# Optimization experiments

Measured on AMD Instinct MI355X. Metric: run time of the kernel, lower is better.

## Reference

```python
import jax, jax.numpy as jnp
import numpy as np

N_NODES = 50000


def _gcn_norm(edge_index, num_nodes):
    # add self-loops (PyG GCNConv default)
    loop = jnp.arange(num_nodes, dtype=edge_index.dtype)
    src = jnp.concatenate([edge_index[0], loop])
    dst = jnp.concatenate([edge_index[1], loop])
    deg = jax.ops.segment_sum(jnp.ones_like(dst, dtype=jnp.float32), dst,
                              num_segments=num_nodes)
    dis = jnp.where(deg > 0, jax.lax.rsqrt(deg), 0.0)  # deg^{-1/2}
    norm = dis[src] * dis[dst]                          # [E+N]
    return src, dst, norm


def _gcn_conv(x, W, b, src, dst, norm, num_nodes):
    h = x @ W                                   # [N, out] transform first
    msg = h[src] * norm[:, None]                # gather + scale  [E+N, out]
    out = jax.ops.segment_sum(msg, dst, num_segments=num_nodes)  # scatter-add
    return out + b


def setup_inputs() -> dict:
    key = jax.random.key(0)
    k1, k2, k3, k4, k5 = jax.random.split(key, 5)
    in_dim, hid_dim, out_dim = 128, 64, 2
    x = jax.random.normal(k1, (N_NODES, in_dim), dtype=jnp.float32)
    edge_index = jax.random.randint(k2, (2, 800000), 0, N_NODES, dtype=jnp.int64)
    s1 = 1.0 / np.sqrt(in_dim)
    s2 = 1.0 / np.sqrt(hid_dim)
    W1 = jax.random.uniform(k3, (in_dim, hid_dim), jnp.float32, -s1, s1)
    b1 = jnp.zeros((hid_dim,), jnp.float32)
    W2 = jax.random.uniform(k4, (hid_dim, hid_dim), jnp.float32, -s2, s2)
    b2 = jnp.zeros((hid_dim,), jnp.float32)
    Wl = jax.random.uniform(k5, (hid_dim, out_dim), jnp.float32, -s2, s2)
    bl = jnp.zeros((out_dim,), jnp.float32)
    return {"x": x, "edge_index": edge_index, "W1": W1, "b1": b1,
            "W2": W2, "b2": b2, "Wl": Wl, "bl": bl}


def reference(x, edge_index, W1, b1, W2, b2, Wl, bl):
    num_nodes = x.shape[0]
    src, dst, norm = _gcn_norm(edge_index, num_nodes)
    h = _gcn_conv(x, W1, b1, src, dst, norm, num_nodes)
    h = jax.nn.relu(h)
    # dropout is identity at inference
    h = _gcn_conv(h, W2, b2, src, dst, norm, num_nodes)
    h = jax.nn.relu(h)
    logits = h @ Wl + bl
    return logits
```

## Files before the change

### kernel.cpp

```cpp
#include <hip/hip_runtime.h>

#define IN_DIM 128
#define HID 64
#define STAGE_CAP 12288

__global__ __launch_bounds__(256) void k_bin_count(const int* __restrict__ dst, int E,
                                                   int* __restrict__ bcnt) {
    __shared__ int h[256];
    int tid = threadIdx.x;
    h[tid] = 0;
    __syncthreads();
    int base = blockIdx.x * 4096;
    int end = min(base + 4096, E);
    for (int i = base + tid; i < end; i += 256) atomicAdd(&h[dst[i] >> 8], 1);
    __syncthreads();
    if (h[tid]) atomicAdd(&bcnt[tid], h[tid]);
}

__global__ __launch_bounds__(256) void k_bucket_scan(const int* __restrict__ bcnt,
                                                     int* __restrict__ bbase,
                                                     int* __restrict__ gcur,
                                                     int* __restrict__ row_start, int N, int E) {
    int tid = threadIdx.x, lane = tid & 63, wid = tid >> 6;
    int v = bcnt[tid], orig = v;
    for (int off = 1; off < 64; off <<= 1) {
        int t = __shfl_up(v, off);
        if (lane >= off) v += t;
    }
    __shared__ int ws[4];
    if (lane == 63) ws[wid] = v;
    __syncthreads();
    int woff = 0;
    for (int w = 0; w < wid; ++w) woff += ws[w];
    bbase[tid] = woff + v - orig;
    gcur[tid] = 0;
    if (tid == 0) row_start[N] = E;
    if (tid == 0) bbase[256] = E;
}

__global__ __launch_bounds__(512) void k_bin_scatter(const int* __restrict__ src,
                                                     const int* __restrict__ dst, int E,
                                                     const int* __restrict__ bbase,
                                                     int* __restrict__ gcur,
                                                     unsigned* __restrict__ ebuf) {
    __shared__ int hist[256];
    __shared__ int gbase[256];
    int tid = threadIdx.x;
    for (int i = tid; i < 256; i += 512) hist[i] = 0;
    __syncthreads();
    int base = blockIdx.x * 4096;
    int pk[8], bkt[8], rnk[8];
#pragma unroll
    for (int i = 0; i < 8; ++i) {
        int e = base + tid + i * 512;
        if (e < E) {
            int s = src[e];
            int d = dst[e];
            bkt[i] = d >> 8;
            pk[i] = ((d & 255) << 16) | s;
            rnk[i] = atomicAdd(&hist[bkt[i]], 1);
        } else {
            bkt[i] = -1;
        }
    }
    __syncthreads();
    for (int b = tid; b < 256; b += 512) {
        int c = hist[b];
        if (c > 0) gbase[b] = bbase[b] + atomicAdd(&gcur[b], c);
    }
    __syncthreads();
#pragma unroll
    for (int i = 0; i < 8; ++i) {
        if (bkt[i] >= 0) ebuf[gbase[bkt[i]] + rnk[i]] = (unsigned)pk[i];
    }
}

__global__ __launch_bounds__(512) void k_bin_sort(const unsigned* __restrict__ ebuf,
                                                  const int* __restrict__ bbase, int N, int E,
                                                  int* __restrict__ row_start,
                                                  float* __restrict__ dis,
                                                  int* __restrict__ csr_src) {
    __shared__ int ldeg[256];
    __shared__ int loff[256];
    __shared__ int lcur[256];
    __shared__ int wsum[8];
    __shared__ unsigned short stage[STAGE_CAP];
    int tid = threadIdx.x;
    int node0 = blockIdx.x << 8;
    int nnode = min(256, N - node0);
    for (int i = tid; i < 256; i += 512) {
        ldeg[i] = 0;
        lcur[i] = 0;
    }
    __syncthreads();
    int bstart = bbase[blockIdx.x];
    int bend = bbase[blockIdx.x + 1];
    int cnt = bend - bstart;
    for (int i = tid; i < cnt; i += 512) {
        unsigned u = ebuf[bstart + i];
        atomicAdd(&ldeg[(u >> 16) & 255], 1);
    }
    __syncthreads();
    int lane = tid & 63, wid = tid >> 6;
    int v = 0, orig = 0;
    if (tid < 256) {
        orig = ldeg[tid];
        v = orig;
    }
    for (int off = 1; off < 64; off <<= 1) {
        int t = __shfl_up(v, off);
        if (lane >= off) v += t;
    }
    if (lane == 63) wsum[wid] = v;
    __syncthreads();
    if (tid < 256) {
        int woff = 0;
        for (int w = 0; w < wid && w < 4; ++w) woff += wsum[w];
        int excl = woff + v - orig;
        loff[tid] = excl;
        if (tid < nnode) {
            row_start[node0 + tid] = bstart + excl;
            dis[node0 + tid] = rsqrtf((float)(orig + 1));
        }
    }
    __syncthreads();
    if (cnt <= STAGE_CAP) {
        for (int i = tid; i < cnt; i += 512) {
            unsigned u = ebuf[bstart + i];
            int dlo = (u >> 16) & 255;
            int pos = loff[dlo] + atomicAdd(&lcur[dlo], 1);
            stage[pos] = (unsigned short)(u & 0xFFFF);
        }
        __syncthreads();
        for (int i = tid; i < cnt; i += 512) csr_src[bstart + i] = (int)stage[i];
    } else {
        for (int i = tid; i < cnt; i += 512) {
            unsigned u = ebuf[bstart + i];
            int dlo = (u >> 16) & 255;
            int pos = bstart + loff[dlo] + atomicAdd(&lcur[dlo], 1);
            csr_src[pos] = (int)(u & 0xFFFF);
        }
    }
}

template <int K>
__global__ __launch_bounds__(256) void k_gemm_scale(const float* __restrict__ X,
                                                    const float* __restrict__ W,
                                                    const float* __restrict__ dis, int N,
                                                    float* __restrict__ out) {
    constexpr int KP = K + 4;
    constexpr int KC = K / 4;
    __shared__ float Xs[64 * KP];
    __shared__ float Ws[K * 64];
    int tid = threadIdx.x;
    int row0 = blockIdx.x * 64;

    const float4* Wg = (const float4*)W;
    float4* Ws4 = (float4*)Ws;
    for (int i = tid; i < K * 16; i += 256) Ws4[i] = Wg[i];
    const float4* Xg = (const float4*)X;
    for (int c = tid; c < 64 * KC; c += 256) {
        int r = c / KC, k4 = c % KC;
        int row = row0 + r;
        float4 vv = make_float4(0.f, 0.f, 0.f, 0.f);
        if (row < N) vv = Xg[(size_t)row * KC + k4];
        *(float4*)&Xs[r * KP + k4 * 4] = vv;
    }
    __syncthreads();

    int cg = tid & 15;
    int rg = tid >> 4;
    float acc[4][4] = {};
#pragma unroll 2
    for (int k = 0; k < K; k += 4) {
        float4 w0 = *(float4*)&Ws[(k + 0) * 64 + cg * 4];
        float4 w1 = *(float4*)&Ws[(k + 1) * 64 + cg * 4];
        float4 w2 = *(float4*)&Ws[(k + 2) * 64 + cg * 4];
        float4 w3 = *(float4*)&Ws[(k + 3) * 64 + cg * 4];
#pragma unroll
        for (int i = 0; i < 4; ++i) {
            float4 xv = *(float4*)&Xs[(rg * 4 + i) * KP + k];
            acc[i][0] += xv.x * w0.x + xv.y * w1.x + xv.z * w2.x + xv.w * w3.x;
            acc[i][1] += xv.x * w0.y + xv.y * w1.y + xv.z * w2.y + xv.w * w3.y;
            acc[i][2] += xv.x * w0.z + xv.y * w1.z + xv.z * w2.z + xv.w * w3.z;
            acc[i][3] += xv.x * w0.w + xv.y * w1.w + xv.z * w2.w + xv.w * w3.w;
        }
    }
#pragma unroll
    for (int i = 0; i < 4; ++i) {
        int row = row0 + rg * 4 + i;
        if (row < N) {
            float s = dis[row];
            *(float4*)&out[(size_t)row * 64 + cg * 4] =
                make_float4(acc[i][0] * s, acc[i][1] * s, acc[i][2] * s, acc[i][3] * s);
        }
    }
}

__global__ __launch_bounds__(256) void k_aggregate(const float* __restrict__ Hs,
                                                   const int* __restrict__ row_start,
                                                   const int* __restrict__ csr_src,
                                                   const float* __restrict__ dis,
                                                   const float* __restrict__ bias, int N,
                                                   float* __restrict__ out) {
    const float4* Hs4 = (const float4*)Hs;
    int wave = threadIdx.x >> 6, lane = threadIdx.x & 63;
    int node = blockIdx.x * 4 + wave;
    if (node >= N) return;
    int t = lane & 7, g = lane >> 3;
    float4 a0 = make_float4(0.f, 0.f, 0.f, 0.f);
    float4 a1 = a0;
    if (g == 0) {
        a0 = Hs4[(size_t)node * 16 + t];
        a1 = Hs4[(size_t)node * 16 + t + 8];
    }
    int e0 = row_start[node], e1 = row_start[node + 1];
    for (int eb = e0; eb < e1; eb += 64) {
        int cnt = min(64, e1 - eb);
        int sv = (eb + lane < e1) ? csr_src[eb + lane] : 0;
        for (int jb = 0; jb < cnt; jb += 16) {
            int i0 = jb + g, i1 = jb + 8 + g;
            int s0 = __shfl(sv, i0 < cnt ? i0 : 0);
            int s1 = __shfl(sv, i1 < cnt ? i1 : 0);
            size_t b0 = (size_t)s0 * 16, b1 = (size_t)s1 * 16;
            float4 z00 = Hs4[b0 + t];
            float4 z01 = Hs4[b0 + t + 8];
            float4 z10 = Hs4[b1 + t];
            float4 z11 = Hs4[b1 + t + 8];
            if (i0 < cnt) {
                a0.x += z00.x; a0.y += z00.y; a0.z += z00.z; a0.w += z00.w;
                a1.x += z01.x; a1.y += z01.y; a1.z += z01.z; a1.w += z01.w;
            }
            if (i1 < cnt) {
                a0.x += z10.x; a0.y += z10.y; a0.z += z10.z; a0.w += z10.w;
                a1.x += z11.x; a1.y += z11.y; a1.z += z11.z; a1.w += z11.w;
            }
        }
    }
#pragma unroll
    for (int off = 8; off < 64; off <<= 1) {
        a0.x += __shfl_xor(a0.x, off); a0.y += __shfl_xor(a0.y, off);
        a0.z += __shfl_xor(a0.z, off); a0.w += __shfl_xor(a0.w, off);
        a1.x += __shfl_xor(a1.x, off); a1.y += __shfl_xor(a1.y, off);
        a1.z += __shfl_xor(a1.z, off); a1.w += __shfl_xor(a1.w, off);
    }
    float sc = dis[node];
    const float4* b4 = (const float4*)bias;
    float4 b0 = b4[t], b1 = b4[t + 8];
    float4 v0, v1;
    v0.x = fmaxf(a0.x * sc + b0.x, 0.f); v0.y = fmaxf(a0.y * sc + b0.y, 0.f);
    v0.z = fmaxf(a0.z * sc + b0.z, 0.f); v0.w = fmaxf(a0.w * sc + b0.w, 0.f);
    v1.x = fmaxf(a1.x * sc + b1.x, 0.f); v1.y = fmaxf(a1.y * sc + b1.y, 0.f);
    v1.z = fmaxf(a1.z * sc + b1.z, 0.f); v1.w = fmaxf(a1.w * sc + b1.w, 0.f);
    if (g == 0) {
        float4* o4 = (float4*)out;
        o4[(size_t)node * 16 + t] = v0;
        o4[(size_t)node * 16 + t + 8] = v1;
    }
}

__global__ __launch_bounds__(256) void k_aggregate_head(const float* __restrict__ Hs,
                                                        const int* __restrict__ row_start,
                                                        const int* __restrict__ csr_src,
                                                        const float* __restrict__ dis,
                                                        const float* __restrict__ bias,
                                                        const float* __restrict__ Wl,
                                                        const float* __restrict__ bl, int N,
                                                        float* __restrict__ out) {
    const float4* Hs4 = (const float4*)Hs;
    int wave = threadIdx.x >> 6, lane = threadIdx.x & 63;
    int node = blockIdx.x * 4 + wave;
    if (node >= N) return;
    int t = lane & 7, g = lane >> 3;
    float4 a0 = make_float4(0.f, 0.f, 0.f, 0.f);
    float4 a1 = a0;
    if (g == 0) {
        a0 = Hs4[(size_t)node * 16 + t];
        a1 = Hs4[(size_t)node * 16 + t + 8];
    }
    int e0 = row_start[node], e1 = row_start[node + 1];
    for (int eb = e0; eb < e1; eb += 64) {
        int cnt = min(64, e1 - eb);
        int sv = (eb + lane < e1) ? csr_src[eb + lane] : 0;
        for (int jb = 0; jb < cnt; jb += 16) {
            int i0 = jb + g, i1 = jb + 8 + g;
            int s0 = __shfl(sv, i0 < cnt ? i0 : 0);
            int s1 = __shfl(sv, i1 < cnt ? i1 : 0);
            size_t b0 = (size_t)s0 * 16, b1 = (size_t)s1 * 16;
            float4 z00 = Hs4[b0 + t];
            float4 z01 = Hs4[b0 + t + 8];
            float4 z10 = Hs4[b1 + t];
            float4 z11 = Hs4[b1 + t + 8];
            if (i0 < cnt) {
                a0.x += z00.x; a0.y += z00.y; a0.z += z00.z; a0.w += z00.w;
                a1.x += z01.x; a1.y += z01.y; a1.z += z01.z; a1.w += z01.w;
            }
            if (i1 < cnt) {
                a0.x += z10.x; a0.y += z10.y; a0.z += z10.z; a0.w += z10.w;
                a1.x += z11.x; a1.y += z11.y; a1.z += z11.z; a1.w += z11.w;
            }
        }
    }
#pragma unroll
    for (int off = 8; off < 64; off <<= 1) {
        a0.x += __shfl_xor(a0.x, off); a0.y += __shfl_xor(a0.y, off);
        a0.z += __shfl_xor(a0.z, off); a0.w += __shfl_xor(a0.w, off);
        a1.x += __shfl_xor(a1.x, off); a1.y += __shfl_xor(a1.y, off);
        a1.z += __shfl_xor(a1.z, off); a1.w += __shfl_xor(a1.w, off);
    }
    float sc = dis[node];
    const float4* b4 = (const float4*)bias;
    float4 b0 = b4[t], b1 = b4[t + 8];
    float4 v0, v1;
    v0.x = fmaxf(a0.x * sc + b0.x, 0.f); v0.y = fmaxf(a0.y * sc + b0.y, 0.f);
    v0.z = fmaxf(a0.z * sc + b0.z, 0.f); v0.w = fmaxf(a0.w * sc + b0.w, 0.f);
    v1.x = fmaxf(a1.x * sc + b1.x, 0.f); v1.y = fmaxf(a1.y * sc + b1.y, 0.f);
    v1.z = fmaxf(a1.z * sc + b1.z, 0.f); v1.w = fmaxf(a1.w * sc + b1.w, 0.f);
    int c0 = 4 * t, c1 = 32 + 4 * t;
    float p0 = v0.x * Wl[(c0 + 0) * 2] + v0.y * Wl[(c0 + 1) * 2] +
               v0.z * Wl[(c0 + 2) * 2] + v0.w * Wl[(c0 + 3) * 2] +
               v1.x * Wl[(c1 + 0) * 2] + v1.y * Wl[(c1 + 1) * 2] +
               v1.z * Wl[(c1 + 2) * 2] + v1.w * Wl[(c1 + 3) * 2];
    float p1 = v0.x * Wl[(c0 + 0) * 2 + 1] + v0.y * Wl[(c0 + 1) * 2 + 1] +
               v0.z * Wl[(c0 + 2) * 2 + 1] + v0.w * Wl[(c0 + 3) * 2 + 1] +
               v1.x * Wl[(c1 + 0) * 2 + 1] + v1.y * Wl[(c1 + 1) * 2 + 1] +
               v1.z * Wl[(c1 + 2) * 2 + 1] + v1.w * Wl[(c1 + 3) * 2 + 1];
    p0 += __shfl_xor(p0, 1); p1 += __shfl_xor(p1, 1);
    p0 += __shfl_xor(p0, 2); p1 += __shfl_xor(p1, 2);
    p0 += __shfl_xor(p0, 4); p1 += __shfl_xor(p1, 4);
    if (lane == 0) {
        out[node * 2 + 0] = p0 + bl[0];
        out[node * 2 + 1] = p1 + bl[1];
    }
}

extern "C" void kernel_launch(void* const* d_in, const int* in_sizes, int n_in,
                              void* d_out, int out_size, void* d_ws, size_t ws_size,
                              hipStream_t stream) {
    const float* x  = (const float*)d_in[0];
    const int*   ei = (const int*)d_in[1];
    const float* W1 = (const float*)d_in[2];
    const float* b1 = (const float*)d_in[3];
    const float* W2 = (const float*)d_in[4];
    const float* b2 = (const float*)d_in[5];
    const float* Wl = (const float*)d_in[6];
    const float* bl = (const float*)d_in[7];

    const int N = in_sizes[0] / IN_DIM;
    const int E = in_sizes[1] / 2;
    const int* src = ei;
    const int* dst = ei + E;

    char* ws = (char*)d_ws;
    size_t off = 0;
    auto alloc = [&](size_t bytes) -> void* {
        void* p = ws + off;
        off = (off + bytes + 255) & ~(size_t)255;
        return p;
    };
    int*   bcnt      = (int*)alloc(256 * 4);
    int*   bbase     = (int*)alloc(257 * 4);
    int*   gcur      = (int*)alloc(256 * 4);
    int*   row_start = (int*)alloc(((size_t)N + 1) * 4);
    float* dis       = (float*)alloc((size_t)N * 4);
    int*   csr_src   = (int*)alloc((size_t)E * 4);
    float* bufA      = (float*)alloc((size_t)N * HID * 4);
    float* bufB      = (float*)alloc((size_t)N * HID * 4);
    unsigned* ebuf   = (unsigned*)bufA;

    hipMemsetAsync(bcnt, 0, 256 * 4, stream);

    int eblk = (E + 4095) / 4096;
    int nb = (N + 255) / 256;
    k_bin_count<<<eblk, 256, 0, stream>>>(dst, E, bcnt);
    k_bucket_scan<<<1, 256, 0, stream>>>(bcnt, bbase, gcur, row_start, N, E);
    k_bin_scatter<<<eblk, 512, 0, stream>>>(src, dst, E, bbase, gcur, ebuf);
    k_bin_sort<<<nb, 512, 0, stream>>>(ebuf, bbase, N, E, row_start, dis, csr_src);

    int gblk = (N + 63) / 64;
    int nblk = (N + 3) / 4;
    k_gemm_scale<IN_DIM><<<gblk, 256, 0, stream>>>(x, W1, dis, N, bufA);
    k_aggregate<<<nblk, 256, 0, stream>>>(bufA, row_start, csr_src, dis, b1, N, bufB);
    k_gemm_scale<HID><<<gblk, 256, 0, stream>>>(bufB, W2, dis, N, bufA);
    k_aggregate_head<<<nblk, 256, 0, stream>>>(bufA, row_start, csr_src, dis, b2, Wl, bl, N,
                                               (float*)d_out);
}
```

Measured before the change: 135.1 us.

## Overlap first-layer GEMM with CSR build by co-scheduling blocks in preprocessing kernels

Removes the dis scaling from the first GEMM so it no longer waits on the degree computation. Its tiles are split across the histogram, scan and scatter kernels, running in spare blocks alongside the edge binning. The per-source normalization moves into the aggregation loop via a gathered dis[src] multiply. The change also replaces the memset and global atomics for the bin count with a per-block 2D histogram, and unrolls aggregation to 4 neighbors per step. In exchange, the aggregation does an extra dis gather per edge, the scan block serially sums eblk rows, and the fused kernels carry larger shared memory.

```diff
diff --git a/kernel.cpp b/kernel.cpp
--- a/kernel.cpp
+++ b/kernel.cpp
@@ -3,75 +3,152 @@
 #define IN_DIM 128
 #define HID 64
 #define STAGE_CAP 12288
-
-__global__ __launch_bounds__(256) void k_bin_count(const int* __restrict__ dst, int E,
-                                                   int* __restrict__ bcnt) {
-    __shared__ int h[256];
+#define SMEM_FLOATS (64 * (IN_DIM + 4) + IN_DIM * 64)
+
+template <int K>
+__device__ __forceinline__ void gemm_body(const float* __restrict__ X,
+                                          const float* __restrict__ W, int N,
+                                          float* __restrict__ out, int blk, float* smem) {
+    constexpr int KP = K + 4;
+    constexpr int KC = K / 4;
+    float* Xs = smem;
+    float* Ws = smem + 64 * KP;
     int tid = threadIdx.x;
-    h[tid] = 0;
+    int row0 = blk * 64;
+
+    const float4* Wg = (const float4*)W;
+    float4* Ws4 = (float4*)Ws;
+    for (int i = tid; i < K * 16; i += 256) Ws4[i] = Wg[i];
+    const float4* Xg = (const float4*)X;
+    for (int c = tid; c < 64 * KC; c += 256) {
+        int r = c / KC, k4 = c % KC;
+        int row = row0 + r;
+        float4 vv = make_float4(0.f, 0.f, 0.f, 0.f);
+        if (row < N) vv = Xg[(size_t)row * KC + k4];
+        *(float4*)&Xs[r * KP + k4 * 4] = vv;
+    }
     __syncthreads();
-    int base = blockIdx.x * 4096;
-    int end = min(base + 4096, E);
-    for (int i = base + tid; i < end; i += 256) atomicAdd(&h[dst[i] >> 8], 1);
-    __syncthreads();
-    if (h[tid]) atomicAdd(&bcnt[tid], h[tid]);
-}
-
-__global__ __launch_bounds__(256) void k_bucket_scan(const int* __restrict__ bcnt,
-                                                     int* __restrict__ bbase,
-                                                     int* __restrict__ gcur,
-                                                     int* __restrict__ row_start, int N, int E) {
-    int tid = threadIdx.x, lane = tid & 63, wid = tid >> 6;
-    int v = bcnt[tid], orig = v;
-    for (int off = 1; off < 64; off <<= 1) {
-        int t = __shfl_up(v, off);
-        if (lane >= off) v += t;
-    }
-    __shared__ int ws[4];
-    if (lane == 63) ws[wid] = v;
-    __syncthreads();
-    int woff = 0;
-    for (int w = 0; w < wid; ++w) woff += ws[w];
-    bbase[tid] = woff + v - orig;
-    gcur[tid] = 0;
-    if (tid == 0) row_start[N] = E;
-    if (tid == 0) bbase[256] = E;
-}
-
-__global__ __launch_bounds__(512) void k_bin_scatter(const int* __restrict__ src,
-                                                     const int* __restrict__ dst, int E,
-                                                     const int* __restrict__ bbase,
-                                                     int* __restrict__ gcur,
-                                                     unsigned* __restrict__ ebuf) {
-    __shared__ int hist[256];
-    __shared__ int gbase[256];
-    int tid = threadIdx.x;
-    for (int i = tid; i < 256; i += 512) hist[i] = 0;
-    __syncthreads();
-    int base = blockIdx.x * 4096;
-    int pk[8], bkt[8], rnk[8];
-#pragma unroll
-    for (int i = 0; i < 8; ++i) {
-        int e = base + tid + i * 512;
-        if (e < E) {
-            int s = src[e];
-            int d = dst[e];
-            bkt[i] = d >> 8;
-            pk[i] = ((d & 255) << 16) | s;
-            rnk[i] = atomicAdd(&hist[bkt[i]], 1);
-        } else {
-            bkt[i] = -1;
-        }
-    }
-    __syncthreads();
-    for (int b = tid; b < 256; b += 512) {
-        int c = hist[b];
-        if (c > 0) gbase[b] = bbase[b] + atomicAdd(&gcur[b], c);
-    }
-    __syncthreads();
-#pragma unroll
-    for (int i = 0; i < 8; ++i) {
-        if (bkt[i] >= 0) ebuf[gbase[bkt[i]] + rnk[i]] = (unsigned)pk[i];
+
+    int cg = tid & 15;
+    int rg = tid >> 4;
+    float acc[4][4] = {};
+#pragma unroll 2
+    for (int k = 0; k < K; k += 4) {
+        float4 w0 = *(float4*)&Ws[(k + 0) * 64 + cg * 4];
+        float4 w1 = *(float4*)&Ws[(k + 1) * 64 + cg * 4];
+        float4 w2 = *(float4*)&Ws[(k + 2) * 64 + cg * 4];
+        float4 w3 = *(float4*)&Ws[(k + 3) * 64 + cg * 4];
+#pragma unroll
+        for (int i = 0; i < 4; ++i) {
+            float4 xv = *(float4*)&Xs[(rg * 4 + i) * KP + k];
+            acc[i][0] += xv.x * w0.x + xv.y * w1.x + xv.z * w2.x + xv.w * w3.x;
+            acc[i][1] += xv.x * w0.y + xv.y * w1.y + xv.z * w2.y + xv.w * w3.y;
+            acc[i][2] += xv.x * w0.z + xv.y * w1.z + xv.z * w2.z + xv.w * w3.z;
+            acc[i][3] += xv.x * w0.w + xv.y * w1.w + xv.z * w2.w + xv.w * w3.w;
+        }
+    }
+#pragma unroll
+    for (int i = 0; i < 4; ++i) {
+        int row = row0 + rg * 4 + i;
+        if (row < N) {
+            *(float4*)&out[(size_t)row * 64 + cg * 4] =
+                make_float4(acc[i][0], acc[i][1], acc[i][2], acc[i][3]);
+        }
+    }
+}
+
+__global__ __launch_bounds__(256) void k_p1(const int* __restrict__ dst, int E, int eblk,
+                                            int* __restrict__ hist2d,
+                                            const float* __restrict__ X,
+                                            const float* __restrict__ W, int N,
+                                            float* __restrict__ out) {
+    __shared__ float smem[SMEM_FLOATS];
+    if ((int)blockIdx.x < eblk) {
+        int* h = (int*)smem;
+        int tid = threadIdx.x;
+        h[tid] = 0;
+        __syncthreads();
+        int base = blockIdx.x * 4096;
+        int end = min(base + 4096, E);
+        for (int i = base + tid; i < end; i += 256) atomicAdd(&h[dst[i] >> 8], 1);
+        __syncthreads();
+        hist2d[blockIdx.x * 256 + tid] = h[tid];
+    } else {
+        gemm_body<IN_DIM>(X, W, N, out, blockIdx.x - eblk, smem);
+    }
+}
+
+__global__ __launch_bounds__(256) void k_p2(const int* __restrict__ hist2d, int eblk,
+                                            int* __restrict__ bbase, int* __restrict__ gcur,
+                                            int* __restrict__ row_start, int N, int E,
+                                            const float* __restrict__ X,
+                                            const float* __restrict__ W,
+                                            float* __restrict__ out, int goff) {
+    __shared__ float smem[SMEM_FLOATS];
+    if (blockIdx.x == 0) {
+        int* wsS = (int*)smem;
+        int tid = threadIdx.x, lane = tid & 63, wid = tid >> 6;
+        int v = 0;
+        for (int k = 0; k < eblk; ++k) v += hist2d[k * 256 + tid];
+        int orig = v;
+        for (int off = 1; off < 64; off <<= 1) {
+            int t = __shfl_up(v, off);
+            if (lane >= off) v += t;
+        }
+        if (lane == 63) wsS[wid] = v;
+        __syncthreads();
+        int woff = 0;
+        for (int w = 0; w < wid; ++w) woff += wsS[w];
+        bbase[tid] = woff + v - orig;
+        gcur[tid] = 0;
+        if (tid == 0) {
+            bbase[256] = E;
+            row_start[N] = E;
+        }
+    } else {
+        gemm_body<IN_DIM>(X, W, N, out, goff + blockIdx.x - 1, smem);
+    }
+}
+
+__global__ __launch_bounds__(256) void k_p3(const int* __restrict__ src,
+                                            const int* __restrict__ dst, int E, int eblk,
+                                            const int* __restrict__ bbase,
+                                            int* __restrict__ gcur, unsigned* __restrict__ ebuf,
+                                            const float* __restrict__ X,
+                                            const float* __restrict__ W, int N,
+                                            float* __restrict__ out, int goff) {
+    __shared__ float smem[SMEM_FLOATS];
+    if ((int)blockIdx.x < eblk) {
+        int* hist = (int*)smem;
+        int* gbase = hist + 256;
+        int tid = threadIdx.x;
+        hist[tid] = 0;
+        __syncthreads();
+        int base = blockIdx.x * 4096;
+        int pk[16], bkt[16], rnk[16];
+#pragma unroll
+        for (int i = 0; i < 16; ++i) {
+            int e = base + tid + i * 256;
+            if (e < E) {
+                int s = src[e];
+                int d = dst[e];
+                bkt[i] = d >> 8;
+                pk[i] = ((d & 255) << 16) | s;
+                rnk[i] = atomicAdd(&hist[bkt[i]], 1);
+            } else {
+                bkt[i] = -1;
+            }
+        }
+        __syncthreads();
+        int c = hist[tid];
+        if (c > 0) gbase[tid] = bbase[tid] + atomicAdd(&gcur[tid], c);
+        __syncthreads();
+#pragma unroll
+        for (int i = 0; i < 16; ++i) {
+            if (bkt[i] >= 0) ebuf[gbase[bkt[i]] + rnk[i]] = (unsigned)pk[i];
+        }
+    } else {
+        gemm_body<IN_DIM>(X, W, N, out, goff + blockIdx.x - eblk, smem);
     }
 }
 
@@ -144,57 +221,11 @@
 }
 
 template <int K>
-__global__ __launch_bounds__(256) void k_gemm_scale(const float* __restrict__ X,
-                                                    const float* __restrict__ W,
-                                                    const float* __restrict__ dis, int N,
-                                                    float* __restrict__ out) {
-    constexpr int KP = K + 4;
-    constexpr int KC = K / 4;
-    __shared__ float Xs[64 * KP];
-    __shared__ float Ws[K * 64];
-    int tid = threadIdx.x;
-    int row0 = blockIdx.x * 64;
-
-    const float4* Wg = (const float4*)W;
-    float4* Ws4 = (float4*)Ws;
-    for (int i = tid; i < K * 16; i += 256) Ws4[i] = Wg[i];
-    const float4* Xg = (const float4*)X;
-    for (int c = tid; c < 64 * KC; c += 256) {
-        int r = c / KC, k4 = c % KC;
-        int row = row0 + r;
-        float4 vv = make_float4(0.f, 0.f, 0.f, 0.f);
-        if (row < N) vv = Xg[(size_t)row * KC + k4];
-        *(float4*)&Xs[r * KP + k4 * 4] = vv;
-    }
-    __syncthreads();
-
-    int cg = tid & 15;
-    int rg = tid >> 4;
-    float acc[4][4] = {};
-#pragma unroll 2
-    for (int k = 0; k < K; k += 4) {
-        float4 w0 = *(float4*)&Ws[(k + 0) * 64 + cg * 4];
-        float4 w1 = *(float4*)&Ws[(k + 1) * 64 + cg * 4];
-        float4 w2 = *(float4*)&Ws[(k + 2) * 64 + cg * 4];
-        float4 w3 = *(float4*)&Ws[(k + 3) * 64 + cg * 4];
-#pragma unroll
-        for (int i = 0; i < 4; ++i) {
-            float4 xv = *(float4*)&Xs[(rg * 4 + i) * KP + k];
-            acc[i][0] += xv.x * w0.x + xv.y * w1.x + xv.z * w2.x + xv.w * w3.x;
-            acc[i][1] += xv.x * w0.y + xv.y * w1.y + xv.z * w2.y + xv.w * w3.y;
-            acc[i][2] += xv.x * w0.z + xv.y * w1.z + xv.z * w2.z + xv.w * w3.z;
-            acc[i][3] += xv.x * w0.w + xv.y * w1.w + xv.z * w2.w + xv.w * w3.w;
-        }
-    }
-#pragma unroll
-    for (int i = 0; i < 4; ++i) {
-        int row = row0 + rg * 4 + i;
-        if (row < N) {
-            float s = dis[row];
-            *(float4*)&out[(size_t)row * 64 + cg * 4] =
-                make_float4(acc[i][0] * s, acc[i][1] * s, acc[i][2] * s, acc[i][3] * s);
-        }
-    }
+__global__ __launch_bounds__(256) void k_gemm(const float* __restrict__ X,
+                                              const float* __restrict__ W, int N,
+                                              float* __restrict__ out) {
+    __shared__ float smem[64 * (K + 4) + K * 64];
+    gemm_body<K>(X, W, N, out, blockIdx.x, smem);
 }
 
 __global__ __launch_bounds__(256) void k_aggregate(const float* __restrict__ Hs,
@@ -208,32 +239,63 @@
     int node = blockIdx.x * 4 + wave;
     if (node >= N) return;
     int t = lane & 7, g = lane >> 3;
+    float dnode = dis[node];
     float4 a0 = make_float4(0.f, 0.f, 0.f, 0.f);
     float4 a1 = a0;
     if (g == 0) {
-        a0 = Hs4[(size_t)node * 16 + t];
-        a1 = Hs4[(size_t)node * 16 + t + 8];
+        float4 s0 = Hs4[(size_t)node * 16 + t];
+        float4 s1 = Hs4[(size_t)node * 16 + t + 8];
+        a0 = make_float4(s0.x * dnode, s0.y * dnode, s0.z * dnode, s0.w * dnode);
+        a1 = make_float4(s1.x * dnode, s1.y * dnode, s1.z * dnode, s1.w * dnode);
     }
     int e0 = row_start[node], e1 = row_start[node + 1];
     for (int eb = e0; eb < e1; eb += 64) {
         int cnt = min(64, e1 - eb);
-        int sv = (eb + lane < e1) ? csr_src[eb + lane] : 0;
-        for (int jb = 0; jb < cnt; jb += 16) {
-            int i0 = jb + g, i1 = jb + 8 + g;
+        int sv = 0;
+        float dv = 0.f;
+        if (eb + lane < e1) {
+            sv = csr_src[eb + lane];
+            dv = dis[sv];
+        }
+        for (int jb = 0; jb < cnt; jb += 32) {
+            int i0 = jb + g, i1 = jb + 8 + g, i2 = jb + 16 + g, i3 = jb + 24 + g;
             int s0 = __shfl(sv, i0 < cnt ? i0 : 0);
             int s1 = __shfl(sv, i1 < cnt ? i1 : 0);
+            int s2 = __shfl(sv, i2 < cnt ? i2 : 0);
+            int s3 = __shfl(sv, i3 < cnt ? i3 : 0);
+            float d0 = __shfl(dv, i0 < cnt ? i0 : 0);
+            float d1 = __shfl(dv, i1 < cnt ? i1 : 0);
+            float d2 = __shfl(dv, i2 < cnt ? i2 : 0);
+            float d3 = __shfl(dv, i3 < cnt ? i3 : 0);
             size_t b0 = (size_t)s0 * 16, b1 = (size_t)s1 * 16;
-            float4 z00 = Hs4[b0 + t];
-            float4 z01 = Hs4[b0 + t + 8];
-            float4 z10 = Hs4[b1 + t];
-            float4 z11 = Hs4[b1 + t + 8];
+            size_t b2 = (size_t)s2 * 16, b3 = (size_t)s3 * 16;
+            float4 z00 = Hs4[b0 + t], z01 = Hs4[b0 + t + 8];
+            float4 z10 = Hs4[b1 + t], z11 = Hs4[b1 + t + 8];
+            float4 z20 = Hs4[b2 + t], z21 = Hs4[b2 + t + 8];
+            float4 z30 = Hs4[b3 + t], z31 = Hs4[b3 + t + 8];
             if (i0 < cnt) {
-                a0.x += z00.x; a0.y += z00.y; a0.z += z00.z; a0.w += z00.w;
-                a1.x += z01.x; a1.y += z01.y; a1.z += z01.z; a1.w += z01.w;
+                a0.x = fmaf(d0, z00.x, a0.x); a0.y = fmaf(d0, z00.y, a0.y);
+                a0.z = fmaf(d0, z00.z, a0.z); a0.w = fmaf(d0, z00.w, a0.w);
+                a1.x = fmaf(d0, z01.x, a1.x); a1.y = fmaf(d0, z01.y, a1.y);
+                a1.z = fmaf(d0, z01.z, a1.z); a1.w = fmaf(d0, z01.w, a1.w);
             }
             if (i1 < cnt) {
-                a0.x += z10.x; a0.y += z10.y; a0.z += z10.z; a0.w += z10.w;
-                a1.x += z11.x; a1.y += z11.y; a1.z += z11.z; a1.w += z11.w;
+                a0.x = fmaf(d1, z10.x, a0.x); a0.y = fmaf(d1, z10.y, a0.y);
+                a0.z = fmaf(d1, z10.z, a0.z); a0.w = fmaf(d1, z10.w, a0.w);
+                a1.x = fmaf(d1, z11.x, a1.x); a1.y = fmaf(d1, z11.y, a1.y);
+                a1.z = fmaf(d1, z11.z, a1.z); a1.w = fmaf(d1, z11.w, a1.w);
+            }
+            if (i2 < cnt) {
+                a0.x = fmaf(d2, z20.x, a0.x); a0.y = fmaf(d2, z20.y, a0.y);
+                a0.z = fmaf(d2, z20.z, a0.z); a0.w = fmaf(d2, z20.w, a0.w);
+                a1.x = fmaf(d2, z21.x, a1.x); a1.y = fmaf(d2, z21.y, a1.y);
+                a1.z = fmaf(d2, z21.z, a1.z); a1.w = fmaf(d2, z21.w, a1.w);
+            }
+            if (i3 < cnt) {
+                a0.x = fmaf(d3, z30.x, a0.x); a0.y = fmaf(d3, z30.y, a0.y);
+                a0.z = fmaf(d3, z30.z, a0.z); a0.w = fmaf(d3, z30.w, a0.w);
+                a1.x = fmaf(d3, z31.x, a1.x); a1.y = fmaf(d3, z31.y, a1.y);
+                a1.z = fmaf(d3, z31.z, a1.z); a1.w = fmaf(d3, z31.w, a1.w);
             }
         }
     }
@@ -244,14 +306,13 @@
         a1.x += __shfl_xor(a1.x, off); a1.y += __shfl_xor(a1.y, off);
         a1.z += __shfl_xor(a1.z, off); a1.w += __shfl_xor(a1.w, off);
     }
-    float sc = dis[node];
     const float4* b4 = (const float4*)bias;
     float4 b0 = b4[t], b1 = b4[t + 8];
     float4 v0, v1;
-    v0.x = fmaxf(a0.x * sc + b0.x, 0.f); v0.y = fmaxf(a0.y * sc + b0.y, 0.f);
-    v0.z = fmaxf(a0.z * sc + b0.z, 0.f); v0.w = fmaxf(a0.w * sc + b0.w, 0.f);
-    v1.x = fmaxf(a1.x * sc + b1.x, 0.f); v1.y = fmaxf(a1.y * sc + b1.y, 0.f);
-    v1.z = fmaxf(a1.z * sc + b1.z, 0.f); v1.w = fmaxf(a1.w * sc + b1.w, 0.f);
+    v0.x = fmaxf(a0.x * dnode + b0.x, 0.f); v0.y = fmaxf(a0.y * dnode + b0.y, 0.f);
+    v0.z = fmaxf(a0.z * dnode + b0.z, 0.f); v0.w = fmaxf(a0.w * dnode + b0.w, 0.f);
+    v1.x = fmaxf(a1.x * dnode + b1.x, 0.f); v1.y = fmaxf(a1.y * dnode + b1.y, 0.f);
+    v1.z = fmaxf(a1.z * dnode + b1.z, 0.f); v1.w = fmaxf(a1.w * dnode + b1.w, 0.f);
     if (g == 0) {
         float4* o4 = (float4*)out;
         o4[(size_t)node * 16 + t] = v0;
@@ -272,32 +333,63 @@
     int node = blockIdx.x * 4 + wave;
     if (node >= N) return;
     int t = lane & 7, g = lane >> 3;
+    float dnode = dis[node];
     float4 a0 = make_float4(0.f, 0.f, 0.f, 0.f);
     float4 a1 = a0;
     if (g == 0) {
-        a0 = Hs4[(size_t)node * 16 + t];
-        a1 = Hs4[(size_t)node * 16 + t + 8];
+        float4 s0 = Hs4[(size_t)node * 16 + t];
+        float4 s1 = Hs4[(size_t)node * 16 + t + 8];
+        a0 = make_float4(s0.x * dnode, s0.y * dnode, s0.z * dnode, s0.w * dnode);
+        a1 = make_float4(s1.x * dnode, s1.y * dnode, s1.z * dnode, s1.w * dnode);
     }
     int e0 = row_start[node], e1 = row_start[node + 1];
     for (int eb = e0; eb < e1; eb += 64) {
         int cnt = min(64, e1 - eb);
-        int sv = (eb + lane < e1) ? csr_src[eb + lane] : 0;
-        for (int jb = 0; jb < cnt; jb += 16) {
-            int i0 = jb + g, i1 = jb + 8 + g;
+        int sv = 0;
+        float dv = 0.f;
+        if (eb + lane < e1) {
+            sv = csr_src[eb + lane];
+            dv = dis[sv];
+        }
+        for (int jb = 0; jb < cnt; jb += 32) {
+            int i0 = jb + g, i1 = jb + 8 + g, i2 = jb + 16 + g, i3 = jb + 24 + g;
             int s0 = __shfl(sv, i0 < cnt ? i0 : 0);
             int s1 = __shfl(sv, i1 < cnt ? i1 : 0);
+            int s2 = __shfl(sv, i2 < cnt ? i2 : 0);
+            int s3 = __shfl(sv, i3 < cnt ? i3 : 0);
+            float d0 = __shfl(dv, i0 < cnt ? i0 : 0);
+            float d1 = __shfl(dv, i1 < cnt ? i1 : 0);
+            float d2 = __shfl(dv, i2 < cnt ? i2 : 0);
+            float d3 = __shfl(dv, i3 < cnt ? i3 : 0);
             size_t b0 = (size_t)s0 * 16, b1 = (size_t)s1 * 16;
-            float4 z00 = Hs4[b0 + t];
-            float4 z01 = Hs4[b0 + t + 8];
-            float4 z10 = Hs4[b1 + t];
-            float4 z11 = Hs4[b1 + t + 8];
+            size_t b2 = (size_t)s2 * 16, b3 = (size_t)s3 * 16;
+            float4 z00 = Hs4[b0 + t], z01 = Hs4[b0 + t + 8];
+            float4 z10 = Hs4[b1 + t], z11 = Hs4[b1 + t + 8];
+            float4 z20 = Hs4[b2 + t], z21 = Hs4[b2 + t + 8];
+            float4 z30 = Hs4[b3 + t], z31 = Hs4[b3 + t + 8];
             if (i0 < cnt) {
-                a0.x += z00.x; a0.y += z00.y; a0.z += z00.z; a0.w += z00.w;
-                a1.x += z01.x; a1.y += z01.y; a1.z += z01.z; a1.w += z01.w;
+                a0.x = fmaf(d0, z00.x, a0.x); a0.y = fmaf(d0, z00.y, a0.y);
+                a0.z = fmaf(d0, z00.z, a0.z); a0.w = fmaf(d0, z00.w, a0.w);
+                a1.x = fmaf(d0, z01.x, a1.x); a1.y = fmaf(d0, z01.y, a1.y);
+                a1.z = fmaf(d0, z01.z, a1.z); a1.w = fmaf(d0, z01.w, a1.w);
             }
             if (i1 < cnt) {
-                a0.x += z10.x; a0.y += z10.y; a0.z += z10.z; a0.w += z10.w;
-                a1.x += z11.x; a1.y += z11.y; a1.z += z11.z; a1.w += z11.w;
+                a0.x = fmaf(d1, z10.x, a0.x); a0.y = fmaf(d1, z10.y, a0.y);
+                a0.z = fmaf(d1, z10.z, a0.z); a0.w = fmaf(d1, z10.w, a0.w);
+                a1.x = fmaf(d1, z11.x, a1.x); a1.y = fmaf(d1, z11.y, a1.y);
+                a1.z = fmaf(d1, z11.z, a1.z); a1.w = fmaf(d1, z11.w, a1.w);
+            }
+            if (i2 < cnt) {
+                a0.x = fmaf(d2, z20.x, a0.x); a0.y = fmaf(d2, z20.y, a0.y);
+                a0.z = fmaf(d2, z20.z, a0.z); a0.w = fmaf(d2, z20.w, a0.w);
+                a1.x = fmaf(d2, z21.x, a1.x); a1.y = fmaf(d2, z21.y, a1.y);
+                a1.z = fmaf(d2, z21.z, a1.z); a1.w = fmaf(d2, z21.w, a1.w);
+            }
+            if (i3 < cnt) {
+                a0.x = fmaf(d3, z30.x, a0.x); a0.y = fmaf(d3, z30.y, a0.y);
+                a0.z = fmaf(d3, z30.z, a0.z); a0.w = fmaf(d3, z30.w, a0.w);
+                a1.x = fmaf(d3, z31.x, a1.x); a1.y = fmaf(d3, z31.y, a1.y);
+                a1.z = fmaf(d3, z31.z, a1.z); a1.w = fmaf(d3, z31.w, a1.w);
             }
         }
     }
@@ -308,14 +400,13 @@
         a1.x += __shfl_xor(a1.x, off); a1.y += __shfl_xor(a1.y, off);
         a1.z += __shfl_xor(a1.z, off); a1.w += __shfl_xor(a1.w, off);
     }
-    float sc = dis[node];
     const float4* b4 = (const float4*)bias;
     float4 b0 = b4[t], b1 = b4[t + 8];
     float4 v0, v1;
-    v0.x = fmaxf(a0.x * sc + b0.x, 0.f); v0.y = fmaxf(a0.y * sc + b0.y, 0.f);
-    v0.z = fmaxf(a0.z * sc + b0.z, 0.f); v0.w = fmaxf(a0.w * sc + b0.w, 0.f);
-    v1.x = fmaxf(a1.x * sc + b1.x, 0.f); v1.y = fmaxf(a1.y * sc + b1.y, 0.f);
-    v1.z = fmaxf(a1.z * sc + b1.z, 0.f); v1.w = fmaxf(a1.w * sc + b1.w, 0.f);
+    v0.x = fmaxf(a0.x * dnode + b0.x, 0.f); v0.y = fmaxf(a0.y * dnode + b0.y, 0.f);
+    v0.z = fmaxf(a0.z * dnode + b0.z, 0.f); v0.w = fmaxf(a0.w * dnode + b0.w, 0.f);
+    v1.x = fmaxf(a1.x * dnode + b1.x, 0.f); v1.y = fmaxf(a1.y * dnode + b1.y, 0.f);
+    v1.z = fmaxf(a1.z * dnode + b1.z, 0.f); v1.w = fmaxf(a1.w * dnode + b1.w, 0.f);
     int c0 = 4 * t, c1 = 32 + 4 * t;
     float p0 = v0.x * Wl[(c0 + 0) * 2] + v0.y * Wl[(c0 + 1) * 2] +
                v0.z * Wl[(c0 + 2) * 2] + v0.w * Wl[(c0 + 3) * 2] +
@@ -358,7 +449,9 @@
         off = (off + bytes + 255) & ~(size_t)255;
         return p;
     };
-    int*   bcnt      = (int*)alloc(256 * 4);
+    const int eblk = (E + 4095) / 4096;
+    const int nb = (N + 255) / 256;
+    int*   hist2d    = (int*)alloc((size_t)eblk * 256 * 4);
     int*   bbase     = (int*)alloc(257 * 4);
     int*   gcur      = (int*)alloc(256 * 4);
     int*   row_start = (int*)alloc(((size_t)N + 1) * 4);
@@ -366,22 +459,22 @@
     int*   csr_src   = (int*)alloc((size_t)E * 4);
     float* bufA      = (float*)alloc((size_t)N * HID * 4);
     float* bufB      = (float*)alloc((size_t)N * HID * 4);
-    unsigned* ebuf   = (unsigned*)bufA;
-
-    hipMemsetAsync(bcnt, 0, 256 * 4, stream);
-
-    int eblk = (E + 4095) / 4096;
-    int nb = (N + 255) / 256;
-    k_bin_count<<<eblk, 256, 0, stream>>>(dst, E, bcnt);
-    k_bucket_scan<<<1, 256, 0, stream>>>(bcnt, bbase, gcur, row_start, N, E);
-    k_bin_scatter<<<eblk, 512, 0, stream>>>(src, dst, E, bbase, gcur, ebuf);
+    unsigned* ebuf   = (unsigned*)bufB;
+
+    const int gblk = (N + 63) / 64;
+    const int g1 = 250, g2 = 250;
+    const int g3 = gblk - g1 - g2;
+
+    k_p1<<<eblk + g1, 256, 0, stream>>>(dst, E, eblk, hist2d, x, W1, N, bufA);
+    k_p2<<<1 + g2, 256, 0, stream>>>(hist2d, eblk, bbase, gcur, row_start, N, E,
+                                     x, W1, bufA, g1);
+    k_p3<<<eblk + g3, 256, 0, stream>>>(src, dst, E, eblk, bbase, gcur, ebuf,
+                                        x, W1, N, bufA, g1 + g2);
     k_bin_sort<<<nb, 512, 0, stream>>>(ebuf, bbase, N, E, row_start, dis, csr_src);
 
-    int gblk = (N + 63) / 64;
     int nblk = (N + 3) / 4;
-    k_gemm_scale<IN_DIM><<<gblk, 256, 0, stream>>>(x, W1, dis, N, bufA);
     k_aggregate<<<nblk, 256, 0, stream>>>(bufA, row_start, csr_src, dis, b1, N, bufB);
-    k_gemm_scale<HID><<<gblk, 256, 0, stream>>>(bufB, W2, dis, N, bufA);
+    k_gemm<HID><<<gblk, 256, 0, stream>>>(bufB, W2, N, bufA);
     k_aggregate_head<<<nblk, 256, 0, stream>>>(bufA, row_start, csr_src, dis, b2, Wl, bl, N,
                                                (float*)d_out);
 }
```

Result: slower. 143.5 us (+6.2%).
